# Performance work log

Measured on AMD Instinct MI355X. Metric: run time of the kernel, lower is better.

The kernel has to match this reference:

```python
import jax, jax.numpy as jnp
import numpy as np

D = 2560
H = 64
HD = D // H  # 40
TE = 512
FF = 4 * D  # 10240
EPS = 1e-5


def _ln(x, eps=EPS):
    # fp32 layernorm, no affine
    x32 = x.astype(jnp.float32)
    mu = jnp.mean(x32, axis=-1, keepdims=True)
    var = jnp.var(x32, axis=-1, keepdims=True)
    return ((x32 - mu) * jax.lax.rsqrt(var + eps)).astype(x.dtype)


def _rope(x, cos, sin):
    # x: [B, H, S_img, HD]; cos/sin: [S_img, HD]
    half = x.shape[-1] // 2
    xr, xi = x[..., :half], x[..., half:]
    x_rot = jnp.concatenate([-xi, xr], axis=-1)
    c = cos[None, None]
    s = sin[None, None]
    return (x.astype(jnp.float32) * c + x_rot.astype(jnp.float32) * s).astype(x.dtype)


def setup_inputs() -> dict:
    key = jax.random.key(0)
    ks = jax.random.split(key, 20)
    f = jnp.float32
    inp = {
        "hidden_states": jax.random.normal(ks[0], (1, 1024, D), f),
        "encoder_hidden_states": jax.random.normal(ks[1], (1, 128, D), f),
        "time_embed": jax.random.normal(ks[2], (1, TE), f),
        "rope_cos": jax.random.uniform(ks[3], (1024, HD), f),
        "rope_sin": jax.random.uniform(ks[4], (1024, HD), f),
        # AdaLayerNormZero linear: time_embed_dim -> 12*D
        "ada_w": jax.random.normal(ks[5], (TE, 12 * D), f) * 0.02,
        "ada_b": jnp.zeros((12 * D,), f),
        # attention projections (stored [in, out])
        "wq": jax.random.normal(ks[6], (D, D), f) * 0.02,
        "bq": jnp.zeros((D,), f),
        "wk": jax.random.normal(ks[7], (D, D), f) * 0.02,
        "bk": jnp.zeros((D,), f),
        "wv": jax.random.normal(ks[8], (D, D), f) * 0.02,
        "bv": jnp.zeros((D,), f),
        "wo": jax.random.normal(ks[9], (D, D), f) * 0.02,
        "bo": jnp.zeros((D,), f),
        # feedforward (shared for img and context streams)
        "w1": jax.random.normal(ks[10], (D, FF), f) * 0.02,
        "b1": jnp.zeros((FF,), f),
        "w2": jax.random.normal(ks[11], (FF, D), f) * 0.02,
        "b2": jnp.zeros((D,), f),
    }
    return inp


def _block(hidden_states, encoder_hidden_states, time_embed, rope_cos, rope_sin,
           ada_w, ada_b, wq, bq, wk, bk, wv, bv, wo, bo, w1, b1, w2, b2):
    B, T, _ = encoder_hidden_states.shape

    # --- AdaLayerNormZero ---
    emb = time_embed @ ada_w + ada_b  # [B, 12*D]
    (shift_msa, c_shift_msa, scale_msa, c_scale_msa, gate_msa, c_gate_msa,
     shift_mlp, c_shift_mlp, scale_mlp, c_scale_mlp, gate_mlp, c_gate_mlp) = jnp.split(emb, 12, axis=1)
    u = lambda v: v[:, None, :]  # [B,1,D]

    norm_h = _ln(hidden_states) * (1 + u(scale_msa)) + u(shift_msa)
    norm_e = _ln(encoder_hidden_states) * (1 + u(c_scale_msa)) + u(c_shift_msa)

    # --- SelfAttention on concatenated [text, image] sequence ---
    x = jnp.concatenate([norm_e, norm_h], axis=1)  # [B,S,D]
    S = x.shape[1]
    def heads(y):
        return y.reshape(B, S, H, HD).transpose(0, 2, 1, 3)  # [B,H,S,HD]
    q = heads(x @ wq + bq)
    k = heads(x @ wk + bk)
    v = heads(x @ wv + bv)
    q = _ln(q)  # fp32 QK-norm over head_dim
    k = _ln(k)
    # partial RoPE on image tokens only
    q = q.at[:, :, T:, :].set(_rope(q[:, :, T:, :], rope_cos, rope_sin))
    k = k.at[:, :, T:, :].set(_rope(k[:, :, T:, :], rope_cos, rope_sin))

    scores = jnp.einsum('bhqd,bhkd->bhqk', q, k) / np.sqrt(HD).astype(np.float32)
    attn = jax.nn.softmax(scores, axis=-1)
    o = jnp.einsum('bhqk,bhkd->bhqd', attn, v)  # [B,H,S,HD]
    o = o.transpose(0, 2, 1, 3).reshape(B, S, D)
    o = o @ wo + bo
    attn_e, attn_h = o[:, :T], o[:, T:]

    # --- residual with attn gates ---
    hidden_states = hidden_states + attn_h * u(gate_msa)
    encoder_hidden_states = encoder_hidden_states + attn_e * u(c_gate_msa)

    # --- MLP with AdaLN modulation + gates ---
    nh = _ln(hidden_states) * (1 + u(scale_mlp)) + u(shift_mlp)
    ne = _ln(encoder_hidden_states) * (1 + u(c_scale_mlp)) + u(c_shift_mlp)
    ff = lambda y: jax.nn.gelu(y @ w1 + b1, approximate=True) @ w2 + b2
    hidden_states = hidden_states + ff(nh) * u(gate_mlp)
    encoder_hidden_states = encoder_hidden_states + ff(ne) * u(c_gate_mlp)
    return hidden_states, encoder_hidden_states


def reference(hidden_states, encoder_hidden_states, time_embed, rope_cos, rope_sin,
              ada_w, ada_b, wq, bq, wk, bk, wv, bv, wo, bo, w1, b1, w2, b2):
    return _block(hidden_states, encoder_hidden_states, time_embed, rope_cos, rope_sin,
                  ada_w, ada_b, wq, bq, wk, bk, wv, bv, wo, bo, w1, b1, w2, b2)
```

## Files before the change

### kernel.cpp

```cpp
#include <hip/hip_runtime.h>
#include <stdint.h>

#define D 2560
#define NH 64
#define HD 40
#define TE_ 512
#define FFD 10240
#define TENC 128
#define THID 1024
#define SEQ 1152

typedef __bf16 bf16_t;
typedef __bf16 bf16x8 __attribute__((ext_vector_type(8)));
typedef float  f32x4  __attribute__((ext_vector_type(4)));

__device__ __forceinline__ void gld_lds16(const void* g, void* l) {
  __builtin_amdgcn_global_load_lds((__attribute__((address_space(1))) void*)(g),
                                   (__attribute__((address_space(3))) void*)(l), 16, 0, 0);
}

__device__ __forceinline__ void wtrans_tile(const float* __restrict__ W, bf16_t* __restrict__ Wt,
                                            int K, int N, int bk, int bn, int tid,
                                            float* tile ) {
  #pragma unroll
  for (int i = 0; i < 4; ++i) {
    int c = i * 256 + tid;
    int r = c >> 4, q = c & 15;
    f32x4 v = *(const f32x4*)(W + (size_t)(bk * 64 + r) * N + bn * 64 + q * 4);
    tile[r * 65 + q * 4 + 0] = v[0]; tile[r * 65 + q * 4 + 1] = v[1];
    tile[r * 65 + q * 4 + 2] = v[2]; tile[r * 65 + q * 4 + 3] = v[3];
  }
  __syncthreads();
  #pragma unroll
  for (int i = 0; i < 2; ++i) {
    int c = i * 256 + tid;
    int n = c >> 3, kc = c & 7;
    bf16x8 o;
    #pragma unroll
    for (int j = 0; j < 8; ++j) o[j] = (bf16_t)tile[(kc * 8 + j) * 65 + n];
    *(bf16x8*)(Wt + (size_t)(bn * 64 + n) * K + bk * 64 + kc * 8) = o;
  }
}

__global__ __launch_bounds__(256) void prep1(
    const float* __restrict__ te, const float* __restrict__ aw, const float* __restrict__ ab,
    float* __restrict__ emb,
    const float* __restrict__ wq, const float* __restrict__ wk, const float* __restrict__ wv,
    bf16_t* __restrict__ wqkvT,
    const float* __restrict__ bq, const float* __restrict__ bk, const float* __restrict__ bv,
    float* __restrict__ bqkv, bf16_t* __restrict__ vt) {
  __shared__ float tile[64 * 65];
  const int b = blockIdx.x, t = threadIdx.x;
  if (b < 120) {
    int j = b * 256 + t;
    float acc = ab[j];
    #pragma unroll 8
    for (int k = 0; k < TE_; ++k) acc = fmaf(te[k], aw[(size_t)k * (12 * D) + j], acc);
    emb[j] = acc;
  } else if (b < 1720) {
    int l = b - 120;  wtrans_tile(wq, wqkvT,                     D, D, l % 40, l / 40, t, tile);
  } else if (b < 3320) {
    int l = b - 1720; wtrans_tile(wk, wqkvT + (size_t)D * D,     D, D, l % 40, l / 40, t, tile);
  } else if (b < 4920) {
    int l = b - 3320; wtrans_tile(wv, wqkvT + (size_t)2 * D * D, D, D, l % 40, l / 40, t, tile);
  } else if (b < 4950) {
    int i = (b - 4920) * 256 + t;
    bqkv[i] = i < D ? bq[i] : (i < 2 * D ? bk[i - D] : bv[i - 2 * D]);
  } else {
    int i = (b - 4950) * 256 + t;
    int h = i / 1152, g = i - h * 1152;
    bf16x8 z = {};
    if (g < 144) {
      #pragma unroll
      for (int j = 0; j < 8; ++j) z[j] = (bf16_t)1.f;
    }
    *(bf16x8*)(vt + ((size_t)h * 48 + 40) * SEQ + g * 8) = z;
  }
}

__global__ void ln_mod(const float* __restrict__ hid, const float* __restrict__ enc,
                       const float* __restrict__ emb, bf16_t* __restrict__ out,
                       int shift_h, int scale_h, int shift_e, int scale_e) {
  int row = blockIdx.x, tid = threadIdx.x;
  const float *src, *sc, *sh;
  if (row < TENC) { src = enc + (size_t)row * D;          sc = emb + scale_e * D; sh = emb + shift_e * D; }
  else            { src = hid + (size_t)(row - TENC) * D; sc = emb + scale_h * D; sh = emb + shift_h * D; }
  float v[10], s = 0.f, s2 = 0.f;
  #pragma unroll
  for (int i = 0; i < 10; ++i) { v[i] = src[tid + i * 256]; s += v[i]; s2 += v[i] * v[i]; }
  #pragma unroll
  for (int o = 32; o > 0; o >>= 1) { s += __shfl_down(s, o); s2 += __shfl_down(s2, o); }
  __shared__ float red[8];
  int wv = tid >> 6, ln = tid & 63;
  if (ln == 0) { red[wv] = s; red[4 + wv] = s2; }
  __syncthreads();
  s  = red[0] + red[1] + red[2] + red[3];
  s2 = red[4] + red[5] + red[6] + red[7];
  float mean = s * (1.f / D);
  float rstd = rsqrtf(s2 * (1.f / D) - mean * mean + 1e-5f);
  #pragma unroll
  for (int i = 0; i < 10; ++i) {
    int c = tid + i * 256;
    out[(size_t)row * D + c] = (bf16_t)((v[i] - mean) * rstd * (1.f + sc[c]) + sh[c]);
  }
}

template<int EPI>
__device__ __forceinline__ void gemm_body(
    bf16_t* As, bf16_t* Bs,
    const bf16_t* __restrict__ A, const bf16_t* __restrict__ Bt,
    const float* __restrict__ bias, int Kld, int ksteps, int N, int nM, int nMN,
    int nwg, int orig,
    bf16_t* __restrict__ outb, float* __restrict__ outp) {
  const int q8 = nwg >> 3, r8 = nwg & 7;
  const int xcd = orig & 7, pos = orig >> 3;
  const int wg = (xcd < r8 ? xcd * (q8 + 1) : r8 * (q8 + 1) + (xcd - r8) * q8) + pos;
  const int part = wg / nMN, rest = wg - part * nMN;
  const int bm = rest % nM, bn = rest / nM;
  const int m0 = bm * 128, n0 = bn * 128;
  const int kbase = part * ksteps;
  const int tid = threadIdx.x, wv = tid >> 6, ln = tid & 63;
  const int wr = wv >> 1, wc = wv & 1, lr = ln & 15, lg = ln >> 4;

  f32x4 acc[4][4];
  const f32x4 zero = {0.f, 0.f, 0.f, 0.f};
  #pragma unroll
  for (int m = 0; m < 4; ++m)
    #pragma unroll
    for (int n = 0; n < 4; ++n) acc[m][n] = zero;

  for (int t = 0; t < ksteps; ++t) {
    const int k0 = (kbase + t) << 6;
    __syncthreads();
    #pragma unroll
    for (int i = 0; i < 4; ++i) {
      int g = wv * 4 + i;
      int s = g * 64 + ln;
      int r = s >> 3, ks = s & 7;
      gld_lds16(A + (size_t)(m0 + r) * Kld + k0 + ((ks ^ (r & 7)) << 3), &As[g * 512]);
    }
    #pragma unroll
    for (int i = 0; i < 4; ++i) {
      int g = wv * 4 + i;
      int s = g * 64 + ln;
      int r = s >> 3, ks = s & 7;
      gld_lds16(Bt + (size_t)(n0 + r) * Kld + k0 + ((ks ^ (r & 7)) << 3), &Bs[g * 512]);
    }
    __syncthreads();
    #pragma unroll
    for (int ks2 = 0; ks2 < 2; ++ks2) {
      int ko = ks2 * 4 + lg;
      bf16x8 af[4], bfr[4];
      #pragma unroll
      for (int m = 0; m < 4; ++m) {
        int r = wr * 64 + m * 16 + lr;
        af[m] = *(const bf16x8*)&As[r * 64 + ((ko ^ (r & 7)) << 3)];
      }
      #pragma unroll
      for (int n = 0; n < 4; ++n) {
        int c = wc * 64 + n * 16 + lr;
        bfr[n] = *(const bf16x8*)&Bs[c * 64 + ((ko ^ (c & 7)) << 3)];
      }
      #pragma unroll
      for (int m = 0; m < 4; ++m)
        #pragma unroll
        for (int n = 0; n < 4; ++n)
          acc[m][n] = __builtin_amdgcn_mfma_f32_16x16x32_bf16(af[m], bfr[n], acc[m][n], 0, 0, 0);
    }
  }

  #pragma unroll
  for (int m = 0; m < 4; ++m) {
    int row = m0 + wr * 64 + m * 16 + (lg << 2);
    #pragma unroll
    for (int n = 0; n < 4; ++n) {
      int col = n0 + wc * 64 + n * 16 + lr;
      float bv = (EPI == 4) ? 0.f : bias[col];
      #pragma unroll
      for (int r = 0; r < 4; ++r) {
        float val = acc[m][n][r] + bv;
        int rr = row + r;
        if (EPI == 1) {
          float z = 0.7978845608028654f * (val + 0.044715f * val * val * val);
          float t2 = 1.f - 2.f / (__expf(2.f * z) + 1.f);
          outb[(size_t)rr * N + col] = (bf16_t)(0.5f * val * (1.f + t2));
        } else {
          outp[(size_t)part * SEQ * N + (size_t)rr * N + col] = val;
        }
      }
    }
  }
}

template<int EPI>
__global__ __launch_bounds__(256, 4) void gemm4(
    const bf16_t* __restrict__ A, const bf16_t* __restrict__ Bt,
    const float* __restrict__ bias, int Kld, int ksteps, int N, int nM, int nMN,
    bf16_t* __restrict__ outb, float* __restrict__ outp) {
  __shared__ bf16_t As[128 * 64];
  __shared__ bf16_t Bs[128 * 64];
  gemm_body<EPI>(As, Bs, A, Bt, bias, Kld, ksteps, N, nM, nMN, gridDim.x, blockIdx.x,
                 outb, outp);
}

__global__ __launch_bounds__(256, 4) void qkv_g(
    const bf16_t* __restrict__ A, const bf16_t* __restrict__ wqkvT,
    float* __restrict__ qparts,
    const float* __restrict__ wo, bf16_t* __restrict__ woT) {
  __shared__ char smem[32768] __attribute__((aligned(16)));
  const int b = blockIdx.x;
  if (b < 1080) {
    gemm_body<4>((bf16_t*)smem, (bf16_t*)(smem + 16384), A, wqkvT, nullptr,
                 D, 20, 3 * D, 9, 540, 1080, b, nullptr, qparts);
  } else {
    int l = b - 1080;
    wtrans_tile(wo, woT, D, D, l % 40, l / 40, threadIdx.x, (float*)smem);
  }
}

__global__ __launch_bounds__(256, 4) void oproj_plus(
    const bf16_t* __restrict__ A, const bf16_t* __restrict__ woT,
    float* __restrict__ oparts,
    const float* __restrict__ w2, bf16_t* __restrict__ w2T) {
  __shared__ char smem[32768] __attribute__((aligned(16)));
  const int b = blockIdx.x;
  if (b < 360) {
    gemm_body<4>((bf16_t*)smem, (bf16_t*)(smem + 16384), A, woT, nullptr,
                 D, 20, D, 9, 180, 360, b, nullptr, oparts);
  } else {
    int l = b - 360;
    wtrans_tile(w2, w2T, FFD, D, l % 160, l / 160, threadIdx.x, (float*)smem);
  }
}

__global__ __launch_bounds__(256) void qkv_red(
    const float* __restrict__ parts, const float* __restrict__ bqkv,
    const float* __restrict__ rc, const float* __restrict__ rs,
    bf16_t* __restrict__ qb, bf16_t* __restrict__ kb, bf16_t* __restrict__ vt) {
  const int r = blockIdx.x, t = threadIdx.x;
  const int h = t >> 2, sub = t & 3;
  __shared__ float cs_s[HD], sn_s[HD];
  const bool rope = (r >= TENC);
  if (rope && t < 2 * HD) {
    if (t < HD) cs_s[t] = rc[(size_t)(r - TENC) * HD + t];
    else        sn_s[t - HD] = rs[(size_t)(r - TENC) * HD + (t - HD)];
  }
  const float* p0 = parts + (size_t)r * (3 * D);
  const float* p1 = p0 + (size_t)SEQ * (3 * D);
  const int cq = h * HD + sub * 10;
  float q[10], k[10], v[10];
  #pragma unroll
  for (int j = 0; j < 10; ++j) {
    q[j] = p0[cq + j] + p1[cq + j] + bqkv[cq + j];
    k[j] = p0[D + cq + j] + p1[D + cq + j] + bqkv[D + cq + j];
    v[j] = p0[2 * D + cq + j] + p1[2 * D + cq + j] + bqkv[2 * D + cq + j];
  }
  __syncthreads();
  float qs = 0.f, qs2 = 0.f, ks = 0.f, ks2 = 0.f;
  #pragma unroll
  for (int j = 0; j < 10; ++j) { qs += q[j]; qs2 += q[j] * q[j]; ks += k[j]; ks2 += k[j] * k[j]; }
  qs += __shfl_xor(qs, 1); qs += __shfl_xor(qs, 2);
  qs2 += __shfl_xor(qs2, 1); qs2 += __shfl_xor(qs2, 2);
  ks += __shfl_xor(ks, 1); ks += __shfl_xor(ks, 2);
  ks2 += __shfl_xor(ks2, 1); ks2 += __shfl_xor(ks2, 2);
  float qm = qs * (1.f / HD), km = ks * (1.f / HD);
  float qr = rsqrtf(qs2 * (1.f / HD) - qm * qm + 1e-5f);
  float kr = rsqrtf(ks2 * (1.f / HD) - km * km + 1e-5f);
  #pragma unroll
  for (int j = 0; j < 10; ++j) { q[j] = (q[j] - qm) * qr; k[j] = (k[j] - km) * kr; }
  if (rope) {
    float pq[10], pk[10];
    #pragma unroll
    for (int j = 0; j < 10; ++j) { pq[j] = __shfl_xor(q[j], 2); pk[j] = __shfl_xor(k[j], 2); }
    #pragma unroll
    for (int j = 0; j < 10; ++j) {
      int d = sub * 10 + j;
      float c = cs_s[d], s = sn_s[d];
      if (d < 20) { q[j] = q[j] * c - pq[j] * s; k[j] = k[j] * c - pk[j] * s; }
      else        { q[j] = q[j] * c + pq[j] * s; k[j] = k[j] * c + pk[j] * s; }
    }
  }
  bf16_t* qd = qb + ((size_t)h * SEQ + r) * 64;
  bf16_t* kd = kb + ((size_t)h * SEQ + r) * 64;
  const float qscale = 0.15811388300841897f;
  #pragma unroll
  for (int j = 0; j < 10; ++j) {
    int d = sub * 10 + j;
    qd[d] = (bf16_t)(q[j] * qscale);
    kd[d] = (bf16_t)k[j];
  }
  #pragma unroll
  for (int j = 0; j < 6; ++j) {
    int d = 40 + sub * 6 + j;
    qd[d] = (bf16_t)0.f; kd[d] = (bf16_t)0.f;
  }
  #pragma unroll
  for (int j = 0; j < 10; ++j) {
    int d = sub * 10 + j;
    vt[((size_t)h * 48 + d) * SEQ + r] = (bf16_t)v[j];
  }
}

template<int P>
__global__ void redk(const float* __restrict__ parts, const float* __restrict__ bias,
                     const float* __restrict__ emb, int gate_h, int gate_e,
                     const float* __restrict__ res_h, const float* __restrict__ res_e,
                     float* __restrict__ out_h, float* __restrict__ out_e) {
  int idx = blockIdx.x * 256 + threadIdx.x;
  int row = idx / (D / 4), col = (idx - row * (D / 4)) * 4;
  f32x4 s = *(const f32x4*)(bias + col);
  #pragma unroll
  for (int p = 0; p < P; ++p)
    s += *(const f32x4*)(parts + (size_t)p * SEQ * D + (size_t)row * D + col);
  const float* res; float* out; int g;
  int r2;
  if (row < TENC) { res = res_e; out = out_e; g = gate_e; r2 = row; }
  else            { res = res_h; out = out_h; g = gate_h; r2 = row - TENC; }
  f32x4 g4 = *(const f32x4*)(emb + (size_t)g * D + col);
  f32x4 rr4 = *(const f32x4*)(res + (size_t)r2 * D + col);
  f32x4 o;
  #pragma unroll
  for (int j = 0; j < 4; ++j) o[j] = rr4[j] + s[j] * g4[j];
  *(f32x4*)(out + (size_t)r2 * D + col) = o;
}

template<int P>
__global__ __launch_bounds__(256) void redk_ln(
    const float* __restrict__ parts, const float* __restrict__ bias,
    const float* __restrict__ emb, int gate_h, int gate_e,
    int shift_h, int scale_h, int shift_e, int scale_e,
    const float* __restrict__ res_h, const float* __restrict__ res_e,
    float* __restrict__ out_h, float* __restrict__ out_e, bf16_t* __restrict__ xout) {
  int row = blockIdx.x, tid = threadIdx.x;
  const float* res; float* out; int g, sh, sc; int r2;
  if (row < TENC) { res = res_e; out = out_e; g = gate_e; sh = shift_e; sc = scale_e; r2 = row; }
  else            { res = res_h; out = out_h; g = gate_h; sh = shift_h; sc = scale_h; r2 = row - TENC; }
  float v[10], s = 0.f, s2 = 0.f;
  #pragma unroll
  for (int i = 0; i < 10; ++i) {
    int c = tid + i * 256;
    float val = bias[c];
    #pragma unroll
    for (int p = 0; p < P; ++p) val += parts[(size_t)p * SEQ * D + (size_t)row * D + c];
    val = res[(size_t)r2 * D + c] + val * emb[(size_t)g * D + c];
    out[(size_t)r2 * D + c] = val;
    v[i] = val; s += val; s2 += val * val;
  }
  #pragma unroll
  for (int o = 32; o > 0; o >>= 1) { s += __shfl_down(s, o); s2 += __shfl_down(s2, o); }
  __shared__ float red[8];
  int wvv = tid >> 6, lnn = tid & 63;
  if (lnn == 0) { red[wvv] = s; red[4 + wvv] = s2; }
  __syncthreads();
  s  = red[0] + red[1] + red[2] + red[3];
  s2 = red[4] + red[5] + red[6] + red[7];
  float mean = s * (1.f / D);
  float rstd = rsqrtf(s2 * (1.f / D) - mean * mean + 1e-5f);
  #pragma unroll
  for (int i = 0; i < 10; ++i) {
    int c = tid + i * 256;
    xout[(size_t)row * D + c] =
        (bf16_t)((v[i] - mean) * rstd * (1.f + emb[(size_t)sc * D + c]) + emb[(size_t)sh * D + c]);
  }
}

__global__ __launch_bounds__(256) void attn_plus(
    const bf16_t* __restrict__ qb, const bf16_t* __restrict__ kb,
    const bf16_t* __restrict__ vt, bf16_t* __restrict__ obf,
    const float* __restrict__ w1, bf16_t* __restrict__ w1T) {
  __shared__ char smem[30720] __attribute__((aligned(16)));
  const int b = blockIdx.x;
  if (b >= 576) {
    int l = b - 576;
    wtrans_tile(w1, w1T, D, FFD, l % 40, l / 40, threadIdx.x, (float*)smem);
    return;
  }
  bf16_t* Ks = (bf16_t*)smem;
  bf16_t* Vs = (bf16_t*)(smem + 8192);
  bf16_t* Ps = (bf16_t*)(smem + 14336);
  const int h = b & 63;
  const int qblk = b >> 6;
  const int tid = threadIdx.x, wv = tid >> 6, ln = tid & 63;
  const int qbase = qblk * 128 + wv * 32;
  const int lr = ln & 15, lg = ln >> 4;

  bf16x8 af[2][2];
  #pragma unroll
  for (int qf = 0; qf < 2; ++qf) {
    const bf16_t* qp = qb + ((size_t)h * SEQ + qbase + qf * 16 + lr) * 64 + lg * 8;
    af[qf][0] = *(const bf16x8*)(qp);
    af[qf][1] = *(const bf16x8*)(qp + 32);
  }
  const f32x4 zero = {0.f, 0.f, 0.f, 0.f};
  f32x4 acc[2][3];
  #pragma unroll
  for (int qf = 0; qf < 2; ++qf) { acc[qf][0] = zero; acc[qf][1] = zero; acc[qf][2] = zero; }

  const bf16_t* kbh = kb + (size_t)h * SEQ * 64;
  const bf16_t* vth = vt + (size_t)h * 48 * SEQ;

  for (int kv0 = 0; kv0 < SEQ; kv0 += 64) {
    __syncthreads();
    #pragma unroll
    for (int i = 0; i < 2; ++i) {
      int g = wv * 2 + i;
      int slot = g * 64 + ln;
      int kr = slot >> 3, so = slot & 7;
      gld_lds16(kbh + (size_t)(kv0 + kr) * 64 + ((so ^ (kr & 7)) << 3), &Ks[g * 512]);
    }
    #pragma unroll
    for (int i = 0; i < 2; ++i) {
      int g = wv + 4 * i;
      if (g < 6) {
        int slot = g * 64 + ln;
        int dr = slot >> 3, so = slot & 7;
        gld_lds16(vth + (size_t)dr * SEQ + kv0 + ((so ^ (dr & 7)) << 3), &Vs[g * 512]);
      }
    }
    __syncthreads();
    #pragma unroll
    for (int nt = 0; nt < 4; ++nt) {
      int kvr = nt * 16 + lr;
      bf16x8 bk0 = *(const bf16x8*)&Ks[kvr * 64 + ((lg ^ (kvr & 7)) << 3)];
      bf16x8 bk1 = *(const bf16x8*)&Ks[kvr * 64 + (((4 + lg) ^ (kvr & 7)) << 3)];
      #pragma unroll
      for (int qf = 0; qf < 2; ++qf) {
        f32x4 s = zero;
        s = __builtin_amdgcn_mfma_f32_16x16x32_bf16(af[qf][0], bk0, s, 0, 0, 0);
        s = __builtin_amdgcn_mfma_f32_16x16x32_bf16(af[qf][1], bk1, s, 0, 0, 0);
        #pragma unroll
        for (int r = 0; r < 4; ++r) {
          float p = exp2f(fmaf(s[r], 1.44269504f, -9.377517766f));
          int q = lg * 4 + r;
          int kv = nt * 16 + lr;
          Ps[(wv * 2 + qf) * 1024 + q * 64 + ((((kv >> 3) ^ (q & 7)) << 3) | (kv & 7))] = (bf16_t)p;
        }
      }
    }
    bf16x8 pa[2][2];
    #pragma unroll
    for (int qf = 0; qf < 2; ++qf)
      #pragma unroll
      for (int kk = 0; kk < 2; ++kk)
        pa[qf][kk] = *(const bf16x8*)&Ps[(wv * 2 + qf) * 1024 + lr * 64 + (((kk * 4 + lg) ^ (lr & 7)) << 3)];
    #pragma unroll
    for (int dt = 0; dt < 3; ++dt) {
      int dr = dt * 16 + lr;
      #pragma unroll
      for (int kk = 0; kk < 2; ++kk) {
        bf16x8 bv = *(const bf16x8*)&Vs[dr * 64 + (((kk * 4 + lg) ^ (dr & 7)) << 3)];
        acc[0][dt] = __builtin_amdgcn_mfma_f32_16x16x32_bf16(pa[0][kk], bv, acc[0][dt], 0, 0, 0);
        acc[1][dt] = __builtin_amdgcn_mfma_f32_16x16x32_bf16(pa[1][kk], bv, acc[1][dt], 0, 0, 0);
      }
    }
  }
  #pragma unroll
  for (int qf = 0; qf < 2; ++qf) {
    float linv[4];
    #pragma unroll
    for (int r = 0; r < 4; ++r)
      linv[r] = 1.f / __shfl(acc[qf][2][r], (ln & 48) | 8);
    #pragma unroll
    for (int dt = 0; dt < 3; ++dt) {
      int d = dt * 16 + lr;
      if (d < HD) {
        #pragma unroll
        for (int r = 0; r < 4; ++r) {
          int q = qbase + qf * 16 + lg * 4 + r;
          obf[(size_t)q * D + h * HD + d] = (bf16_t)(acc[qf][dt][r] * linv[r]);
        }
      }
    }
  }
}

extern "C" void kernel_launch(void* const* d_in, const int* in_sizes, int n_in,
                              void* d_out, int out_size, void* d_ws, size_t ws_size,
                              hipStream_t stream) {
  const float* hid = (const float*)d_in[0];
  const float* enc = (const float*)d_in[1];
  const float* tem = (const float*)d_in[2];
  const float* rc  = (const float*)d_in[3];
  const float* rs  = (const float*)d_in[4];
  const float* aw  = (const float*)d_in[5];
  const float* ab  = (const float*)d_in[6];
  const float* wq  = (const float*)d_in[7];
  const float* bq  = (const float*)d_in[8];
  const float* wk  = (const float*)d_in[9];
  const float* bk  = (const float*)d_in[10];
  const float* wvv = (const float*)d_in[11];
  const float* bv  = (const float*)d_in[12];
  const float* wo  = (const float*)d_in[13];
  const float* bo  = (const float*)d_in[14];
  const float* w1  = (const float*)d_in[15];
  const float* b1  = (const float*)d_in[16];
  const float* w2  = (const float*)d_in[17];
  const float* b2  = (const float*)d_in[18];
  float* out_hid = (float*)d_out;
  float* out_enc = out_hid + (size_t)THID * D;

  char* ws = (char*)d_ws;
  size_t off = 0;
  auto alloc = [&](size_t b) { char* p = ws + off; off += (b + 255) & ~(size_t)255; return p; };
  float*  emb  = (float*) alloc((size_t)12 * D * 4);
  bf16_t* xln  = (bf16_t*)alloc((size_t)SEQ * D * 2);
  bf16_t* aff  = (bf16_t*)alloc((size_t)SEQ * FFD * 2);
  bf16_t* vt   = (bf16_t*)alloc((size_t)NH * 48 * SEQ * 2);
  bf16_t* qbb  = (bf16_t*)alloc((size_t)NH * SEQ * 64 * 2);
  bf16_t* kbb  = (bf16_t*)alloc((size_t)NH * SEQ * 64 * 2);
  bf16_t* wqkvT= (bf16_t*)alloc((size_t)3 * D * D * 2);
  bf16_t* woT  = (bf16_t*)alloc((size_t)D * D * 2);
  bf16_t* w1T  = (bf16_t*)alloc((size_t)FFD * D * 2);
  bf16_t* w2T  = (bf16_t*)alloc((size_t)D * FFD * 2);
  float*  bqkv = (float*) alloc((size_t)3 * D * 4);
  bf16_t* obf = xln;
  float*  h1  = (float*)qbb;
  float*  e1  = h1 + (size_t)THID * D;
  float*  qparts = (float*)w1T;
  float*  oparts = (float*)wqkvT;
  float*  fparts = (float*)wqkvT;

  prep1<<<dim3(5238), dim3(256), 0, stream>>>(tem, aw, ab, emb, wq, wk, wvv,
      wqkvT, bq, bk, bv, bqkv, vt);
  ln_mod<<<dim3(SEQ), dim3(256), 0, stream>>>(hid, enc, emb, xln, 0, 2, 1, 3);
  qkv_g<<<dim3(2680), dim3(256), 0, stream>>>(xln, wqkvT, qparts, wo, woT);
  qkv_red<<<dim3(SEQ), dim3(256), 0, stream>>>(qparts, bqkv, rc, rs, qbb, kbb, vt);
  attn_plus<<<dim3(6976), dim3(256), 0, stream>>>(qbb, kbb, vt, obf, w1, w1T);
  oproj_plus<<<dim3(6760), dim3(256), 0, stream>>>(obf, woT, oparts, w2, w2T);
  redk_ln<2><<<dim3(SEQ), dim3(256), 0, stream>>>(oparts, bo, emb, 4, 5, 6, 8, 7, 9,
      hid, enc, h1, e1, xln);
  gemm4<1><<<dim3(720), dim3(256), 0, stream>>>(xln, w1T, b1, D, 40, FFD, 9, 720,
      aff, nullptr);
  gemm4<4><<<dim3(720), dim3(256), 0, stream>>>(aff, w2T, nullptr, FFD, 40, D, 9, 180,
      nullptr, fparts);
  redk<4><<<dim3(2880), dim3(256), 0, stream>>>(fparts, b2, emb, 10, 11, h1, e1, out_hid, out_enc);
}
```

Before: 442.2 us.

## Split ada GEMV into K-parallel kernel and fuse weight transpose into LN kernel

The AdaLN GEMV moves out of the prep kernel into its own kernel. Each block now covers 64 outputs with the K dimension split across four waves and reduced in LDS, which gives 480 blocks instead of 120 blocks each doing a serial 512-long loop. The QKV weight transpose, bias packing and vt padding work is merged into the layernorm-modulation kernel, so that work runs alongside the LN rows instead of in the kernel the LN had to wait on. This removes the long serial GEMV tail from the critical path, but it adds a larger mixed-role kernel whose LN blocks now share LDS with the transpose tile.

```diff
diff --git a/kernel.cpp b/kernel.cpp
--- a/kernel.cpp
+++ b/kernel.cpp
@@ -42,60 +42,71 @@
   }
 }
 
-__global__ __launch_bounds__(256) void prep1(
-    const float* __restrict__ te, const float* __restrict__ aw, const float* __restrict__ ab,
-    float* __restrict__ emb,
+__global__ __launch_bounds__(256) void ada_g(
+    const float* __restrict__ te, const float* __restrict__ aw,
+    const float* __restrict__ ab, float* __restrict__ emb) {
+  __shared__ float red[4][64];
+  const int t = threadIdx.x;
+  const int j = blockIdx.x * 64 + (t & 63);
+  const int kc = t >> 6;
+  const float* awp = aw + (size_t)(kc * 128) * (12 * D) + j;
+  const float* tep = te + kc * 128;
+  float a0 = 0.f, a1 = 0.f, a2 = 0.f, a3 = 0.f;
+  #pragma unroll 8
+  for (int k = 0; k < 128; k += 4) {
+    a0 = fmaf(tep[k],     awp[(size_t)k * (12 * D)],       a0);
+    a1 = fmaf(tep[k + 1], awp[(size_t)(k + 1) * (12 * D)], a1);
+    a2 = fmaf(tep[k + 2], awp[(size_t)(k + 2) * (12 * D)], a2);
+    a3 = fmaf(tep[k + 3], awp[(size_t)(k + 3) * (12 * D)], a3);
+  }
+  red[kc][t & 63] = (a0 + a1) + (a2 + a3);
+  __syncthreads();
+  if (t < 64)
+    emb[j] = ab[j] + red[0][t] + red[1][t] + red[2][t] + red[3][t];
+}
+
+__global__ __launch_bounds__(256) void ln_plus(
+    const float* __restrict__ hid, const float* __restrict__ enc,
+    const float* __restrict__ emb, bf16_t* __restrict__ out,
     const float* __restrict__ wq, const float* __restrict__ wk, const float* __restrict__ wv,
     bf16_t* __restrict__ wqkvT,
     const float* __restrict__ bq, const float* __restrict__ bk, const float* __restrict__ bv,
     float* __restrict__ bqkv, bf16_t* __restrict__ vt) {
   __shared__ float tile[64 * 65];
-  const int b = blockIdx.x, t = threadIdx.x;
-  if (b < 120) {
-    int j = b * 256 + t;
-    float acc = ab[j];
-    #pragma unroll 8
-    for (int k = 0; k < TE_; ++k) acc = fmaf(te[k], aw[(size_t)k * (12 * D) + j], acc);
-    emb[j] = acc;
-  } else if (b < 1720) {
-    int l = b - 120;  wtrans_tile(wq, wqkvT,                     D, D, l % 40, l / 40, t, tile);
-  } else if (b < 3320) {
-    int l = b - 1720; wtrans_tile(wk, wqkvT + (size_t)D * D,     D, D, l % 40, l / 40, t, tile);
-  } else if (b < 4920) {
-    int l = b - 3320; wtrans_tile(wv, wqkvT + (size_t)2 * D * D, D, D, l % 40, l / 40, t, tile);
-  } else if (b < 4950) {
-    int i = (b - 4920) * 256 + t;
-    bqkv[i] = i < D ? bq[i] : (i < 2 * D ? bk[i - D] : bv[i - 2 * D]);
-  } else {
-    int i = (b - 4950) * 256 + t;
-    int h = i / 1152, g = i - h * 1152;
-    bf16x8 z = {};
-    if (g < 144) {
-      #pragma unroll
-      for (int j = 0; j < 8; ++j) z[j] = (bf16_t)1.f;
-    }
-    *(bf16x8*)(vt + ((size_t)h * 48 + 40) * SEQ + g * 8) = z;
-  }
-}
-
-__global__ void ln_mod(const float* __restrict__ hid, const float* __restrict__ enc,
-                       const float* __restrict__ emb, bf16_t* __restrict__ out,
-                       int shift_h, int scale_h, int shift_e, int scale_e) {
-  int row = blockIdx.x, tid = threadIdx.x;
+  const int b = blockIdx.x, tid = threadIdx.x;
+  if (b >= 1152) {
+    if (b < 2752)      { int l = b - 1152; wtrans_tile(wq, wqkvT,                     D, D, l % 40, l / 40, tid, tile); }
+    else if (b < 4352) { int l = b - 2752; wtrans_tile(wk, wqkvT + (size_t)D * D,     D, D, l % 40, l / 40, tid, tile); }
+    else if (b < 5952) { int l = b - 4352; wtrans_tile(wv, wqkvT + (size_t)2 * D * D, D, D, l % 40, l / 40, tid, tile); }
+    else if (b < 5982) {
+      int i = (b - 5952) * 256 + tid;
+      bqkv[i] = i < D ? bq[i] : (i < 2 * D ? bk[i - D] : bv[i - 2 * D]);
+    } else {
+      int i = (b - 5982) * 256 + tid;
+      int h = i / 1152, g = i - h * 1152;
+      bf16x8 z = {};
+      if (g < 144) {
+        #pragma unroll
+        for (int j = 0; j < 8; ++j) z[j] = (bf16_t)1.f;
+      }
+      *(bf16x8*)(vt + ((size_t)h * 48 + 40) * SEQ + g * 8) = z;
+    }
+    return;
+  }
+  const int row = b;
   const float *src, *sc, *sh;
-  if (row < TENC) { src = enc + (size_t)row * D;          sc = emb + scale_e * D; sh = emb + shift_e * D; }
-  else            { src = hid + (size_t)(row - TENC) * D; sc = emb + scale_h * D; sh = emb + shift_h * D; }
+  if (row < TENC) { src = enc + (size_t)row * D;          sc = emb + 3 * D; sh = emb + 1 * D; }
+  else            { src = hid + (size_t)(row - TENC) * D; sc = emb + 2 * D; sh = emb + 0 * D; }
   float v[10], s = 0.f, s2 = 0.f;
   #pragma unroll
   for (int i = 0; i < 10; ++i) { v[i] = src[tid + i * 256]; s += v[i]; s2 += v[i] * v[i]; }
   #pragma unroll
   for (int o = 32; o > 0; o >>= 1) { s += __shfl_down(s, o); s2 += __shfl_down(s2, o); }
-  __shared__ float red[8];
-  int wv = tid >> 6, ln = tid & 63;
-  if (ln == 0) { red[wv] = s; red[4 + wv] = s2; }
+  int wv2 = tid >> 6, ln = tid & 63;
+  if (ln == 0) { tile[wv2] = s; tile[4 + wv2] = s2; }
   __syncthreads();
-  s  = red[0] + red[1] + red[2] + red[3];
-  s2 = red[4] + red[5] + red[6] + red[7];
+  s  = tile[0] + tile[1] + tile[2] + tile[3];
+  s2 = tile[4] + tile[5] + tile[6] + tile[7];
   float mean = s * (1.f / D);
   float rstd = rsqrtf(s2 * (1.f / D) - mean * mean + 1e-5f);
   #pragma unroll
@@ -520,9 +531,9 @@
   float*  oparts = (float*)wqkvT;
   float*  fparts = (float*)wqkvT;
 
-  prep1<<<dim3(5238), dim3(256), 0, stream>>>(tem, aw, ab, emb, wq, wk, wvv,
-      wqkvT, bq, bk, bv, bqkv, vt);
-  ln_mod<<<dim3(SEQ), dim3(256), 0, stream>>>(hid, enc, emb, xln, 0, 2, 1, 3);
+  ada_g<<<dim3(480), dim3(256), 0, stream>>>(tem, aw, ab, emb);
+  ln_plus<<<dim3(6270), dim3(256), 0, stream>>>(hid, enc, emb, xln,
+      wq, wk, wvv, wqkvT, bq, bk, bv, bqkv, vt);
   qkv_g<<<dim3(2680), dim3(256), 0, stream>>>(xln, wqkvT, qparts, wo, woT);
   qkv_red<<<dim3(SEQ), dim3(256), 0, stream>>>(qparts, bqkv, rc, rs, qbb, kbb, vt);
   attn_plus<<<dim3(6976), dim3(256), 0, stream>>>(qbb, kbb, vt, obf, w1, w1T);
```

Measured after the change: 424.9 us. -3.9%, faster.
